# Performance work log

Hardware: AMD Instinct MI355X
Metric: run time of the kernel (lower is better)

The kernel has to match this reference:

```python
import jax, jax.numpy as jnp
import numpy as np

# Sparse grid constants (closed over; coords live on this grid)
B, H, W = 2, 640, 640
N = 409600
CIN, CH, COUT = 64, 64, 64
K = 3
PAD = (K - 1) // 2


def setup_inputs() -> dict:
    key = jax.random.key(0)
    ks = jax.random.split(key, 6)
    # unique active coordinates via permutation of the dense grid
    lin = jax.random.permutation(ks[0], B * H * W)[:N]
    b = lin // (H * W)
    rem = lin % (H * W)
    coords = jnp.stack([b, rem // W, rem % W], axis=1).astype(jnp.int32)  # [N,3]
    features = jax.random.normal(ks[1], (N, CIN), jnp.float32)
    w1 = jax.random.normal(ks[2], (K, K, CIN, CH), jnp.float32) * (1.0 / np.sqrt(K * K * CIN))
    b1 = jnp.zeros((CH,), jnp.float32)
    w2 = jax.random.normal(ks[3], (K, K, CH, COUT), jnp.float32) * (1.0 / np.sqrt(K * K * CH))
    b2 = jnp.zeros((COUT,), jnp.float32)
    wd = jax.random.normal(ks[4], (CIN, COUT), jnp.float32) * (1.0 / np.sqrt(CIN))
    return {"features": features, "coords": coords, "w1": w1, "b1": b1,
            "w2": w2, "b2": b2, "wd": wd}


def _build_grid(coords):
    # dense hash: grid[b,y,x] = row index into features, -1 if inactive
    grid = jnp.full((B, H, W), -1, dtype=jnp.int32)
    return grid.at[coords[:, 0], coords[:, 1], coords[:, 2]].set(
        jnp.arange(N, dtype=jnp.int32))


def _subm_conv(feat, coords, grid, w, bias):
    # Submanifold conv: out only at active sites; gather-matmul-accumulate per offset.
    cb, cy, cx = coords[:, 0], coords[:, 1], coords[:, 2]
    out = jnp.zeros((N, w.shape[-1]), feat.dtype)
    for ky in range(K):              # small fixed kernel loop (rulebook offsets)
        for kx in range(K):
            dy, dx = ky - PAD, kx - PAD
            ny, nx = cy + dy, cx + dx
            inb = (ny >= 0) & (ny < H) & (nx >= 0) & (nx < W)
            nidx = grid[cb, jnp.clip(ny, 0, H - 1), jnp.clip(nx, 0, W - 1)]
            valid = inb & (nidx >= 0)
            g = feat[jnp.where(valid, nidx, 0)]          # [N, Cin] gather
            g = jnp.where(valid[:, None], g, 0.0)
            out = out + g @ w[ky, kx]                    # per-offset GEMM
    if bias is not None:
        out = out + bias
    return out


def reference(features, coords, w1, b1, w2, b2, wd):
    grid = _build_grid(coords)
    out = jax.nn.relu(_subm_conv(features, coords, grid, w1, b1))
    out = jax.nn.relu(_subm_conv(out, coords, grid, w2, b2))
    residual = features @ wd                  # 1x1 subm conv, no bias
    out = jax.nn.relu(out + residual)         # sparse_add: identical index sets
    return out
```

## Files before the change

### kernel.cpp

```cpp
#include <hip/hip_runtime.h>
#include <hip/hip_bf16.h>
#include <stdint.h>

#define NP 409600
#define HG 640
#define WG 640
#define HW (HG*WG)

typedef __bf16 bf16x8 __attribute__((ext_vector_type(8)));
typedef float f32x4 __attribute__((ext_vector_type(4)));


__global__ void scatter_kernel(const int* __restrict__ coords, int* __restrict__ grid) {
    int i = blockIdx.x * 256 + threadIdx.x;
    int b = coords[3*i], y = coords[3*i+1], x = coords[3*i+2];
    grid[b*HW + y*WG + x] = i;
}

__global__ void nbr_kernel(const int* __restrict__ coords, const int* __restrict__ grid,
                           int* __restrict__ nbr) {
    int i = blockIdx.x * 256 + threadIdx.x;
    int b = coords[3*i], y = coords[3*i+1], x = coords[3*i+2];
    int baseg = b*HW;
    #pragma unroll
    for (int t = 0; t < 9; ++t) {
        int ny = y + t/3 - 1, nx = x + t%3 - 1;
        int g = -1;
        if (ny >= 0 && ny < HG && nx >= 0 && nx < WG)
            g = grid[baseg + ny*WG + nx];
        nbr[t*NP + i] = g;
    }
}

__global__ void cast_feat_kernel(const float* __restrict__ f, __hip_bfloat16* __restrict__ fb) {
    long i = (long)(blockIdx.x * 256 + threadIdx.x) * 8;
    float4 a = *(const float4*)(f + i);
    float4 b = *(const float4*)(f + i + 4);
    union { uint4 q; __hip_bfloat16 h[8]; } u;
    u.h[0] = __float2bfloat16(a.x); u.h[1] = __float2bfloat16(a.y);
    u.h[2] = __float2bfloat16(a.z); u.h[3] = __float2bfloat16(a.w);
    u.h[4] = __float2bfloat16(b.x); u.h[5] = __float2bfloat16(b.y);
    u.h[6] = __float2bfloat16(b.z); u.h[7] = __float2bfloat16(b.w);
    *(uint4*)(fb + i) = u.q;
}

__global__ void cast_w_kernel(const float* __restrict__ w1, const float* __restrict__ w2,
                              const float* __restrict__ wd,
                              __hip_bfloat16* __restrict__ wc1, __hip_bfloat16* __restrict__ wc2) {
    int i = blockIdx.x * 256 + threadIdx.x;
    if (i < 9*4096) {
        int t = i >> 12, r = i & 4095, n = r >> 6, k = r & 63;
        wc1[i] = __float2bfloat16(w1[(t << 12) + (k << 6) + n]);
    }
    int j = i - 9*4096;
    if (j >= 0 && j < 10*4096) {
        int t = j >> 12, r = j & 4095, n = r >> 6, k = r & 63;
        float v = (t < 9) ? w2[(t << 12) + (k << 6) + n] : wd[(k << 6) + n];
        wc2[j] = __float2bfloat16(v);
    }
}


#define LDA 72
#define LDB 72

template<int NTAP, bool FINAL>
__launch_bounds__(256)
__global__ void conv_kernel(const __hip_bfloat16* __restrict__ src,
                            const __hip_bfloat16* __restrict__ idsrc,
                            const int* __restrict__ nbr,
                            const __hip_bfloat16* __restrict__ wT,
                            const float* __restrict__ bias,
                            __hip_bfloat16* __restrict__ out_bf,
                            float* __restrict__ out_f) {
    __shared__ __align__(16) __hip_bfloat16 As[128 * LDA];
    __shared__ __align__(16) __hip_bfloat16 Bs[64 * LDB];

    const int tid  = threadIdx.x;
    const int base = blockIdx.x * 128;
    const int wave = tid >> 6, lane = tid & 63;
    const int srow = tid >> 1, shalf = tid & 1;

    f32x4 acc[2][4];
    f32x4 accR[2][4];
    #pragma unroll
    for (int i = 0; i < 2; ++i)
        #pragma unroll
        for (int j = 0; j < 4; ++j) {
            acc[i][j]  = (f32x4){0.f, 0.f, 0.f, 0.f};
            accR[i][j] = (f32x4){0.f, 0.f, 0.f, 0.f};
        }

    for (int t = 0; t < NTAP; ++t) {
        if (t) __syncthreads();

        int g;
        const __hip_bfloat16* sp;
        if (FINAL && t == NTAP - 1) { g = base + srow; sp = idsrc; }
        else                        { g = nbr[t*NP + base + srow]; sp = src; }
        uint4 v0, v1, v2, v3;
        if (g >= 0) {
            const uint4* p = (const uint4*)(sp + (long)g*64 + shalf*32);
            v0 = p[0]; v1 = p[1]; v2 = p[2]; v3 = p[3];
        } else {
            v0 = v1 = v2 = v3 = make_uint4(0u, 0u, 0u, 0u);
        }
        uint4* dst = (uint4*)(As + srow*LDA + shalf*32);
        dst[0] = v0; dst[1] = v1; dst[2] = v2; dst[3] = v3;

        const uint4* wp = (const uint4*)(wT + t*4096);
        #pragma unroll
        for (int j = 0; j < 2; ++j) {
            int e = tid + j*256;
            int l = e * 8;
            int n = l >> 6, k = l & 63;
            *(uint4*)(Bs + n*LDB + k) = wp[e];
        }
        __syncthreads();

        auto do_mfma = [&](f32x4 (&ac)[2][4]) {
            #pragma unroll
            for (int ks = 0; ks < 2; ++ks) {
                int kb = ks*32 + (lane >> 4)*8;
                bf16x8 a0 = *(const bf16x8*)(As + (wave*32      + (lane & 15))*LDA + kb);
                bf16x8 a1 = *(const bf16x8*)(As + (wave*32 + 16 + (lane & 15))*LDA + kb);
                bf16x8 b0 = *(const bf16x8*)(Bs + ( 0 + (lane & 15))*LDB + kb);
                bf16x8 b1 = *(const bf16x8*)(Bs + (16 + (lane & 15))*LDB + kb);
                bf16x8 b2 = *(const bf16x8*)(Bs + (32 + (lane & 15))*LDB + kb);
                bf16x8 b3 = *(const bf16x8*)(Bs + (48 + (lane & 15))*LDB + kb);
                ac[0][0] = __builtin_amdgcn_mfma_f32_16x16x32_bf16(a0, b0, ac[0][0], 0, 0, 0);
                ac[0][1] = __builtin_amdgcn_mfma_f32_16x16x32_bf16(a0, b1, ac[0][1], 0, 0, 0);
                ac[0][2] = __builtin_amdgcn_mfma_f32_16x16x32_bf16(a0, b2, ac[0][2], 0, 0, 0);
                ac[0][3] = __builtin_amdgcn_mfma_f32_16x16x32_bf16(a0, b3, ac[0][3], 0, 0, 0);
                ac[1][0] = __builtin_amdgcn_mfma_f32_16x16x32_bf16(a1, b0, ac[1][0], 0, 0, 0);
                ac[1][1] = __builtin_amdgcn_mfma_f32_16x16x32_bf16(a1, b1, ac[1][1], 0, 0, 0);
                ac[1][2] = __builtin_amdgcn_mfma_f32_16x16x32_bf16(a1, b2, ac[1][2], 0, 0, 0);
                ac[1][3] = __builtin_amdgcn_mfma_f32_16x16x32_bf16(a1, b3, ac[1][3], 0, 0, 0);
            }
        };
        if (FINAL && t == NTAP - 1) do_mfma(accR);
        else                        do_mfma(acc);
    }

    const int col = lane & 15, quad = lane >> 4;
    #pragma unroll
    for (int cb = 0; cb < 4; ++cb) {
        float bv = bias[cb*16 + col];
        #pragma unroll
        for (int mb = 0; mb < 2; ++mb) {
            #pragma unroll
            for (int r = 0; r < 4; ++r) {
                float v = acc[mb][cb][r] + bv;
                v = v > 0.f ? v : 0.f;
                long row = base + wave*32 + mb*16 + quad*4 + r;
                int  c   = cb*16 + col;
                if (FINAL) {
                    v += accR[mb][cb][r];
                    v = v > 0.f ? v : 0.f;
                    out_f[row*64 + c] = v;
                } else {
                    out_bf[row*64 + c] = __float2bfloat16(v);
                }
            }
        }
    }
}


extern "C" void kernel_launch(void* const* d_in, const int* in_sizes, int n_in,
                              void* d_out, int out_size, void* d_ws, size_t ws_size,
                              hipStream_t stream) {
    const float* features = (const float*)d_in[0];
    const int*   coords   = (const int*)d_in[1];
    const float* w1 = (const float*)d_in[2];
    const float* b1 = (const float*)d_in[3];
    const float* w2 = (const float*)d_in[4];
    const float* b2 = (const float*)d_in[5];
    const float* wd = (const float*)d_in[6];
    float* out = (float*)d_out;

    char* ws = (char*)d_ws;
    int*            grid = (int*)ws;
    int*            nbr  = (int*)(ws + 3276800);
    __hip_bfloat16* fb   = (__hip_bfloat16*)(ws + 18022400);
    __hip_bfloat16* y1   = (__hip_bfloat16*)(ws + 70451200);
    __hip_bfloat16* wc1  = (__hip_bfloat16*)(ws + 122880000);
    __hip_bfloat16* wc2  = (__hip_bfloat16*)(ws + 122953728);

    hipMemsetAsync(grid, 0xFF, (size_t)HW * 2 * sizeof(int), stream);

    scatter_kernel  <<<1600,  256, 0, stream>>>(coords, grid);
    cast_feat_kernel<<<12800, 256, 0, stream>>>(features, fb);
    cast_w_kernel   <<<304,   256, 0, stream>>>(w1, w2, wd, wc1, wc2);
    nbr_kernel      <<<1600,  256, 0, stream>>>(coords, grid, nbr);

    conv_kernel<9,  false><<<3200, 256, 0, stream>>>(fb, fb, nbr, wc1, b1, y1, nullptr);
    conv_kernel<10, true ><<<3200, 256, 0, stream>>>(y1, fb, nbr, wc2, b2, nullptr, out);
}
```

Before: 344.6 us.

## Sort active sites into spatial tiles and gather fp32 features directly in conv

Active sites are bucketed into 16x16 spatial tiles with a histogram, a prefix scan and an atomic scatter. The neighbor table and conv blocks are then built in this locality order, and outputs are written back through the order permutation, so gathered neighbor rows tend to be cache-resident. The separate fp32-to-bf16 feature cast pass is removed, and the first conv and the residual path now read fp32 features and convert them while staging. Block IDs are also swizzled across XCDs and launch bounds raised. The trade-offs are extra preprocessing kernels with atomics, a single-block scan, fp32 gathers that move twice the bytes, and scattered output writes.

```diff
diff --git a/kernel.cpp b/kernel.cpp
--- a/kernel.cpp
+++ b/kernel.cpp
@@ -6,6 +6,9 @@
 #define HG 640
 #define WG 640
 #define HW (HG*WG)
+#define TDIM 16
+#define TPB  40
+#define NTILE 3200
 
 typedef __bf16 bf16x8 __attribute__((ext_vector_type(8)));
 typedef float f32x4 __attribute__((ext_vector_type(4)));
@@ -17,10 +20,57 @@
     grid[b*HW + y*WG + x] = i;
 }
 
-__global__ void nbr_kernel(const int* __restrict__ coords, const int* __restrict__ grid,
-                           int* __restrict__ nbr) {
+__global__ void hist_kernel(const int* __restrict__ coords, int* __restrict__ hist) {
     int i = blockIdx.x * 256 + threadIdx.x;
     int b = coords[3*i], y = coords[3*i+1], x = coords[3*i+2];
+    atomicAdd(&hist[b*(TPB*TPB) + (y>>4)*TPB + (x>>4)], 1);
+}
+
+__global__ void scan_kernel(int* __restrict__ hist) {
+    __shared__ int part[256];
+    int t = threadIdx.x;
+    int loc[13];
+    int s = 0;
+    #pragma unroll
+    for (int k = 0; k < 13; ++k) {
+        int idx = t*13 + k;
+        int v = (idx < NTILE) ? hist[idx] : 0;
+        loc[k] = s; s += v;
+    }
+    part[t] = s;
+    __syncthreads();
+    for (int off = 1; off < 256; off <<= 1) {
+        int v = (t >= off) ? part[t - off] : 0;
+        __syncthreads();
+        part[t] += v;
+        __syncthreads();
+    }
+    int pre = (t > 0) ? part[t-1] : 0;
+    #pragma unroll
+    for (int k = 0; k < 13; ++k) {
+        int idx = t*13 + k;
+        if (idx < NTILE) hist[idx] = pre + loc[k];
+    }
+}
+
+__global__ void ord_kernel(const int* __restrict__ coords, int* __restrict__ offs,
+                           int* __restrict__ ord, int* __restrict__ lsort) {
+    int i = blockIdx.x * 256 + threadIdx.x;
+    int b = coords[3*i], y = coords[3*i+1], x = coords[3*i+2];
+    int tile = b*(TPB*TPB) + (y>>4)*TPB + (x>>4);
+    int pos = atomicAdd(&offs[tile], 1);
+    ord[pos]   = i;
+    lsort[pos] = b*HW + y*WG + x;
+}
+
+__global__ void nbr_kernel(const int* __restrict__ lsort, const int* __restrict__ grid,
+                           int* __restrict__ nbrp) {
+    int j = blockIdx.x * 256 + threadIdx.x;
+    int lin = lsort[j];
+    int b = lin / HW;
+    int rem = lin - b*HW;
+    int y = rem / WG;
+    int x = rem - y*WG;
     int baseg = b*HW;
     #pragma unroll
     for (int t = 0; t < 9; ++t) {
@@ -28,20 +78,8 @@
         int g = -1;
         if (ny >= 0 && ny < HG && nx >= 0 && nx < WG)
             g = grid[baseg + ny*WG + nx];
-        nbr[t*NP + i] = g;
-    }
-}
-
-__global__ void cast_feat_kernel(const float* __restrict__ f, __hip_bfloat16* __restrict__ fb) {
-    long i = (long)(blockIdx.x * 256 + threadIdx.x) * 8;
-    float4 a = *(const float4*)(f + i);
-    float4 b = *(const float4*)(f + i + 4);
-    union { uint4 q; __hip_bfloat16 h[8]; } u;
-    u.h[0] = __float2bfloat16(a.x); u.h[1] = __float2bfloat16(a.y);
-    u.h[2] = __float2bfloat16(a.z); u.h[3] = __float2bfloat16(a.w);
-    u.h[4] = __float2bfloat16(b.x); u.h[5] = __float2bfloat16(b.y);
-    u.h[6] = __float2bfloat16(b.z); u.h[7] = __float2bfloat16(b.w);
-    *(uint4*)(fb + i) = u.q;
+        nbrp[t*NP + j] = g;
+    }
 }
 
 __global__ void cast_w_kernel(const float* __restrict__ w1, const float* __restrict__ w2,
@@ -64,11 +102,12 @@
 #define LDA 72
 #define LDB 72
 
-template<int NTAP, bool FINAL>
-__launch_bounds__(256)
-__global__ void conv_kernel(const __hip_bfloat16* __restrict__ src,
-                            const __hip_bfloat16* __restrict__ idsrc,
-                            const int* __restrict__ nbr,
+template<bool SRC32, bool FINAL>
+__launch_bounds__(256, 4)
+__global__ void conv_kernel(const void* __restrict__ srcv,
+                            const float* __restrict__ idsrc,
+                            const int* __restrict__ nbrp,
+                            const int* __restrict__ ord,
                             const __hip_bfloat16* __restrict__ wT,
                             const float* __restrict__ bias,
                             __hip_bfloat16* __restrict__ out_bf,
@@ -76,10 +115,13 @@
     __shared__ __align__(16) __hip_bfloat16 As[128 * LDA];
     __shared__ __align__(16) __hip_bfloat16 Bs[64 * LDB];
 
-    const int tid  = threadIdx.x;
-    const int base = blockIdx.x * 128;
+    const int tid = threadIdx.x;
+    const int sbid = (blockIdx.x & 7) * 400 + (blockIdx.x >> 3);
+    const int base = sbid * 128;
     const int wave = tid >> 6, lane = tid & 63;
     const int srow = tid >> 1, shalf = tid & 1;
+
+    const int rrow = ord[base + srow];
 
     f32x4 acc[2][4];
     f32x4 accR[2][4];
@@ -91,13 +133,18 @@
             accR[i][j] = (f32x4){0.f, 0.f, 0.f, 0.f};
         }
 
-    for (int t = 0; t < NTAP; ++t) {
-        if (t) __syncthreads();
-
-        int g;
-        const __hip_bfloat16* sp;
-        if (FINAL && t == NTAP - 1) { g = base + srow; sp = idsrc; }
-        else                        { g = nbr[t*NP + base + srow]; sp = src; }
+    auto stageB = [&](int t) {
+        const uint4* wp = (const uint4*)(wT + t*4096);
+        #pragma unroll
+        for (int jj = 0; jj < 2; ++jj) {
+            int e = tid + jj*256;
+            int l = e * 8;
+            int n = l >> 6, k = l & 63;
+            *(uint4*)(Bs + n*LDB + k) = wp[e];
+        }
+    };
+
+    auto stage_bf = [&](const __hip_bfloat16* sp, int g) {
         uint4 v0, v1, v2, v3;
         if (g >= 0) {
             const uint4* p = (const uint4*)(sp + (long)g*64 + shalf*32);
@@ -107,42 +154,79 @@
         }
         uint4* dst = (uint4*)(As + srow*LDA + shalf*32);
         dst[0] = v0; dst[1] = v1; dst[2] = v2; dst[3] = v3;
-
-        const uint4* wp = (const uint4*)(wT + t*4096);
-        #pragma unroll
-        for (int j = 0; j < 2; ++j) {
-            int e = tid + j*256;
-            int l = e * 8;
-            int n = l >> 6, k = l & 63;
-            *(uint4*)(Bs + n*LDB + k) = wp[e];
-        }
-        __syncthreads();
-
-        auto do_mfma = [&](f32x4 (&ac)[2][4]) {
-            #pragma unroll
-            for (int ks = 0; ks < 2; ++ks) {
-                int kb = ks*32 + (lane >> 4)*8;
-                bf16x8 a0 = *(const bf16x8*)(As + (wave*32      + (lane & 15))*LDA + kb);
-                bf16x8 a1 = *(const bf16x8*)(As + (wave*32 + 16 + (lane & 15))*LDA + kb);
-                bf16x8 b0 = *(const bf16x8*)(Bs + ( 0 + (lane & 15))*LDB + kb);
-                bf16x8 b1 = *(const bf16x8*)(Bs + (16 + (lane & 15))*LDB + kb);
-                bf16x8 b2 = *(const bf16x8*)(Bs + (32 + (lane & 15))*LDB + kb);
-                bf16x8 b3 = *(const bf16x8*)(Bs + (48 + (lane & 15))*LDB + kb);
-                ac[0][0] = __builtin_amdgcn_mfma_f32_16x16x32_bf16(a0, b0, ac[0][0], 0, 0, 0);
-                ac[0][1] = __builtin_amdgcn_mfma_f32_16x16x32_bf16(a0, b1, ac[0][1], 0, 0, 0);
-                ac[0][2] = __builtin_amdgcn_mfma_f32_16x16x32_bf16(a0, b2, ac[0][2], 0, 0, 0);
-                ac[0][3] = __builtin_amdgcn_mfma_f32_16x16x32_bf16(a0, b3, ac[0][3], 0, 0, 0);
-                ac[1][0] = __builtin_amdgcn_mfma_f32_16x16x32_bf16(a1, b0, ac[1][0], 0, 0, 0);
-                ac[1][1] = __builtin_amdgcn_mfma_f32_16x16x32_bf16(a1, b1, ac[1][1], 0, 0, 0);
-                ac[1][2] = __builtin_amdgcn_mfma_f32_16x16x32_bf16(a1, b2, ac[1][2], 0, 0, 0);
-                ac[1][3] = __builtin_amdgcn_mfma_f32_16x16x32_bf16(a1, b3, ac[1][3], 0, 0, 0);
+    };
+
+    auto stage_f32 = [&](const float* sp, int g) {
+        uint4* dst = (uint4*)(As + srow*LDA + shalf*32);
+        #pragma unroll
+        for (int h = 0; h < 2; ++h) {
+            float4 f0, f1, f2, f3;
+            if (g >= 0) {
+                const float4* p = (const float4*)(sp + (long)g*64 + shalf*32 + h*16);
+                f0 = p[0]; f1 = p[1]; f2 = p[2]; f3 = p[3];
+            } else {
+                f0 = f1 = f2 = f3 = make_float4(0.f, 0.f, 0.f, 0.f);
             }
-        };
-        if (FINAL && t == NTAP - 1) do_mfma(accR);
-        else                        do_mfma(acc);
+            union { uint4 q; __hip_bfloat16 hh[8]; } u0, u1;
+            u0.hh[0] = __float2bfloat16(f0.x); u0.hh[1] = __float2bfloat16(f0.y);
+            u0.hh[2] = __float2bfloat16(f0.z); u0.hh[3] = __float2bfloat16(f0.w);
+            u0.hh[4] = __float2bfloat16(f1.x); u0.hh[5] = __float2bfloat16(f1.y);
+            u0.hh[6] = __float2bfloat16(f1.z); u0.hh[7] = __float2bfloat16(f1.w);
+            u1.hh[0] = __float2bfloat16(f2.x); u1.hh[1] = __float2bfloat16(f2.y);
+            u1.hh[2] = __float2bfloat16(f2.z); u1.hh[3] = __float2bfloat16(f2.w);
+            u1.hh[4] = __float2bfloat16(f3.x); u1.hh[5] = __float2bfloat16(f3.y);
+            u1.hh[6] = __float2bfloat16(f3.z); u1.hh[7] = __float2bfloat16(f3.w);
+            dst[h*2]     = u0.q;
+            dst[h*2 + 1] = u1.q;
+        }
+    };
+
+    auto do_mfma = [&](f32x4 (&ac)[2][4]) {
+        #pragma unroll
+        for (int ks = 0; ks < 2; ++ks) {
+            int kb = ks*32 + (lane >> 4)*8;
+            bf16x8 a0 = *(const bf16x8*)(As + (wave*32      + (lane & 15))*LDA + kb);
+            bf16x8 a1 = *(const bf16x8*)(As + (wave*32 + 16 + (lane & 15))*LDA + kb);
+            bf16x8 b0 = *(const bf16x8*)(Bs + ( 0 + (lane & 15))*LDB + kb);
+            bf16x8 b1 = *(const bf16x8*)(Bs + (16 + (lane & 15))*LDB + kb);
+            bf16x8 b2 = *(const bf16x8*)(Bs + (32 + (lane & 15))*LDB + kb);
+            bf16x8 b3 = *(const bf16x8*)(Bs + (48 + (lane & 15))*LDB + kb);
+            ac[0][0] = __builtin_amdgcn_mfma_f32_16x16x32_bf16(a0, b0, ac[0][0], 0, 0, 0);
+            ac[0][1] = __builtin_amdgcn_mfma_f32_16x16x32_bf16(a0, b1, ac[0][1], 0, 0, 0);
+            ac[0][2] = __builtin_amdgcn_mfma_f32_16x16x32_bf16(a0, b2, ac[0][2], 0, 0, 0);
+            ac[0][3] = __builtin_amdgcn_mfma_f32_16x16x32_bf16(a0, b3, ac[0][3], 0, 0, 0);
+            ac[1][0] = __builtin_amdgcn_mfma_f32_16x16x32_bf16(a1, b0, ac[1][0], 0, 0, 0);
+            ac[1][1] = __builtin_amdgcn_mfma_f32_16x16x32_bf16(a1, b1, ac[1][1], 0, 0, 0);
+            ac[1][2] = __builtin_amdgcn_mfma_f32_16x16x32_bf16(a1, b2, ac[1][2], 0, 0, 0);
+            ac[1][3] = __builtin_amdgcn_mfma_f32_16x16x32_bf16(a1, b3, ac[1][3], 0, 0, 0);
+        }
+    };
+
+    for (int t = 0; t < 9; ++t) {
+        if (t) __syncthreads();
+        int g = nbrp[t*NP + base + srow];
+        if (SRC32) stage_f32((const float*)srcv, g);
+        else       stage_bf ((const __hip_bfloat16*)srcv, g);
+        stageB(t);
+        __syncthreads();
+        do_mfma(acc);
+    }
+    if (FINAL) {
+        __syncthreads();
+        stage_f32(idsrc, rrow);
+        stageB(9);
+        __syncthreads();
+        do_mfma(accR);
     }
 
     const int col = lane & 15, quad = lane >> 4;
+    int rowid[2][4];
+    #pragma unroll
+    for (int mb = 0; mb < 2; ++mb)
+        #pragma unroll
+        for (int r = 0; r < 4; ++r)
+            rowid[mb][r] = ord[base + wave*32 + mb*16 + quad*4 + r];
+
     #pragma unroll
     for (int cb = 0; cb < 4; ++cb) {
         float bv = bias[cb*16 + col];
@@ -152,7 +236,7 @@
             for (int r = 0; r < 4; ++r) {
                 float v = acc[mb][cb][r] + bv;
                 v = v > 0.f ? v : 0.f;
-                long row = base + wave*32 + mb*16 + quad*4 + r;
+                long row = rowid[mb][r];
                 int  c   = cb*16 + col;
                 if (FINAL) {
                     v += accR[mb][cb][r];
@@ -180,20 +264,27 @@
     float* out = (float*)d_out;
 
     char* ws = (char*)d_ws;
-    int*            grid = (int*)ws;
-    int*            nbr  = (int*)(ws + 3276800);
-    __hip_bfloat16* fb   = (__hip_bfloat16*)(ws + 18022400);
-    __hip_bfloat16* y1   = (__hip_bfloat16*)(ws + 70451200);
-    __hip_bfloat16* wc1  = (__hip_bfloat16*)(ws + 122880000);
-    __hip_bfloat16* wc2  = (__hip_bfloat16*)(ws + 122953728);
+    int*            grid  = (int*)ws;
+    int*            nbrp  = (int*)(ws + 3276800);
+    __hip_bfloat16* y1    = (__hip_bfloat16*)(ws + 18022400);
+    __hip_bfloat16* wc1   = (__hip_bfloat16*)(ws + 70451200);
+    __hip_bfloat16* wc2   = (__hip_bfloat16*)(ws + 70524928);
+    int*            ord   = (int*)(ws + 70606848);
+    int*            lsort = (int*)(ws + 72245248);
+    int*            hist  = (int*)(ws + 73883648);
 
     hipMemsetAsync(grid, 0xFF, (size_t)HW * 2 * sizeof(int), stream);
-
-    scatter_kernel  <<<1600,  256, 0, stream>>>(coords, grid);
-    cast_feat_kernel<<<12800, 256, 0, stream>>>(features, fb);
-    cast_w_kernel   <<<304,   256, 0, stream>>>(w1, w2, wd, wc1, wc2);
-    nbr_kernel      <<<1600,  256, 0, stream>>>(coords, grid, nbr);
-
-    conv_kernel<9,  false><<<3200, 256, 0, stream>>>(fb, fb, nbr, wc1, b1, y1, nullptr);
-    conv_kernel<10, true ><<<3200, 256, 0, stream>>>(y1, fb, nbr, wc2, b2, nullptr, out);
-}
+    hipMemsetAsync(hist, 0x00, (size_t)NTILE * sizeof(int), stream);
+
+    scatter_kernel<<<1600, 256, 0, stream>>>(coords, grid);
+    hist_kernel   <<<1600, 256, 0, stream>>>(coords, hist);
+    scan_kernel   <<<1,    256, 0, stream>>>(hist);
+    ord_kernel    <<<1600, 256, 0, stream>>>(coords, hist, ord, lsort);
+    cast_w_kernel <<<304,  256, 0, stream>>>(w1, w2, wd, wc1, wc2);
+    nbr_kernel    <<<1600, 256, 0, stream>>>(lsort, grid, nbrp);
+
+    conv_kernel<true,  false><<<3200, 256, 0, stream>>>((const void*)features, nullptr,
+                                                        nbrp, ord, wc1, b1, y1, nullptr);
+    conv_kernel<false, true ><<<3200, 256, 0, stream>>>((const void*)y1, features,
+                                                        nbrp, ord, wc2, b2, nullptr, out);
+}
```

Measured after the change: 447.6 us. 29.9% more time.
